# Optimization experiments

Hardware: AMD Instinct MI355X
Metric: run time of the kernel (lower is better)

## Reference

```python
import jax, jax.numpy as jnp
import numpy as np

N_NODES = 500000
N_EDGES = 5000000


def _sage_conv(x, edge_index, Wl, bl, Wr):
    # PyG SAGEConv (aggr='mean', root_weight=True):
    #   out = lin_l(mean_{j in N(i)} x_j) + lin_r(x_i)
    # edge_index[0] = source, edge_index[1] = target
    src, dst = edge_index[0], edge_index[1]
    n = x.shape[0]
    msg = x[src]  # [E, F] gather
    agg = jax.ops.segment_sum(msg, dst, num_segments=n)  # [N, F]
    deg = jax.ops.segment_sum(jnp.ones((src.shape[0],), x.dtype), dst, num_segments=n)
    agg = agg / jnp.maximum(deg, 1.0)[:, None]  # mean aggregation
    return agg @ Wl.T + bl + x @ Wr.T


def setup_inputs() -> dict:
    key = jax.random.key(0)
    k1, k2, k3, k4, k5, k6 = jax.random.split(key, 6)
    x = jax.random.normal(k1, (N_NODES, 2), dtype=jnp.float32)
    edge_index = jax.random.randint(k2, (2, N_EDGES), 0, N_NODES, dtype=jnp.int64)
    # conv1: SAGEConv(2, 16); conv2: SAGEConv(16, 1)
    s1 = 1.0 / np.sqrt(2.0)
    s2 = 1.0 / np.sqrt(16.0)
    W1l = jax.random.uniform(k3, (16, 2), jnp.float32, -s1, s1)
    W1r = jax.random.uniform(k4, (16, 2), jnp.float32, -s1, s1)
    b1 = jnp.zeros((16,), jnp.float32)
    W2l = jax.random.uniform(k5, (1, 16), jnp.float32, -s2, s2)
    W2r = jax.random.uniform(k6, (1, 16), jnp.float32, -s2, s2)
    b2 = jnp.zeros((1,), jnp.float32)
    return {"x": x, "edge_index": edge_index,
            "W1l": W1l, "b1": b1, "W1r": W1r,
            "W2l": W2l, "b2": b2, "W2r": W2r}


def reference(x, edge_index, W1l, b1, W1r, W2l, b2, W2r):
    h = jax.nn.relu(_sage_conv(x, edge_index, W1l, b1, W1r))  # [N, 16]
    h = _sage_conv(h, edge_index, W2l, b2, W2r)               # [N, 1]
    return jax.nn.sigmoid(h).squeeze(-1)                      # [N]
```

## Files before the change

kernel.cpp:

```cpp
#include <hip/hip_runtime.h>


static constexpr int ABLOCK = 512;
static constexpr int PBLOCK = 1024;
static constexpr int PGRID = 256;
static constexpr int BUCKET_BITS = 9;
static constexpr int BUCKET_NODES = 1 << BUCKET_BITS;
static constexpr int MAXNB = 1024;
static constexpr int CAP = 8192;
static constexpr int CSTRIDE = 16;
static constexpr int MAXCHUNK = 19584;

static constexpr float S1 = 65536.0f;
static constexpr float IS1 = 1.0f / 65536.0f;
static constexpr long long B1 = 8LL * 65536LL;
static constexpr float S2 = 16384.0f;
static constexpr float IS2 = 1.0f / 16384.0f;

__global__ __launch_bounds__(512) void k_init(unsigned* __restrict__ cursor, int NB) {
    int b = blockIdx.x * 512 + threadIdx.x;
    if (b < NB) cursor[(size_t)b * CSTRIDE] = (unsigned)b * (unsigned)CAP;
}

__global__ __launch_bounds__(PBLOCK) void k_part(
    const int* __restrict__ src, const int* __restrict__ dst,
    unsigned* __restrict__ cursor, unsigned* __restrict__ entries,
    int E, int NB)
{
    __shared__ unsigned sorted[MAXCHUNK];
    __shared__ unsigned hist[MAXNB];
    __shared__ unsigned loc[MAXNB];
    __shared__ unsigned base[MAXNB];
    const int tid = threadIdx.x;
    int chunk = ((E + (int)gridDim.x - 1) / (int)gridDim.x + 3) & ~3;
    const int e0 = blockIdx.x * chunk;
    const int e1 = min(e0 + chunk, E);
    const int n = max(0, e1 - e0);
    const int nv = n >> 2;
    const int4* dst4 = reinterpret_cast<const int4*>(dst + e0);
    const int4* src4 = reinterpret_cast<const int4*>(src + e0);

    for (int b = tid; b < MAXNB; b += PBLOCK) hist[b] = 0;
    __syncthreads();

    for (int t = tid; t < nv; t += PBLOCK) {
        int4 d = dst4[t];
        atomicAdd(&hist[(unsigned)d.x >> BUCKET_BITS], 1u);
        atomicAdd(&hist[(unsigned)d.y >> BUCKET_BITS], 1u);
        atomicAdd(&hist[(unsigned)d.z >> BUCKET_BITS], 1u);
        atomicAdd(&hist[(unsigned)d.w >> BUCKET_BITS], 1u);
    }
    for (int e = e0 + (nv << 2) + tid; e < e1; e += PBLOCK)
        atomicAdd(&hist[(unsigned)dst[e] >> BUCKET_BITS], 1u);
    __syncthreads();

    if (tid < NB) loc[tid] = hist[tid];
    __syncthreads();
    for (int off = 1; off < NB; off <<= 1) {
        unsigned v = 0;
        if (tid < NB && tid >= off) v = loc[tid - off];
        __syncthreads();
        if (tid < NB) loc[tid] += v;
        __syncthreads();
    }
    if (tid < NB) loc[tid] -= hist[tid];

    if (tid < NB) {
        int b = tid + (int)(blockIdx.x % (unsigned)NB);
        if (b >= NB) b -= NB;
        base[b] = atomicAdd(&cursor[(size_t)b * CSTRIDE], hist[b]);
    }
    __syncthreads();
    for (int b = tid; b < MAXNB; b += PBLOCK) hist[b] = 0;
    __syncthreads();

    for (int t = tid; t < nv; t += PBLOCK) {
        int4 d = dst4[t];
        int4 s = src4[t];
        {
            unsigned bk = (unsigned)d.x >> BUCKET_BITS;
            unsigned r = atomicAdd(&hist[bk], 1u);
            sorted[loc[bk] + r] = ((unsigned)s.x << BUCKET_BITS) | ((unsigned)d.x & (BUCKET_NODES - 1));
        }
        {
            unsigned bk = (unsigned)d.y >> BUCKET_BITS;
            unsigned r = atomicAdd(&hist[bk], 1u);
            sorted[loc[bk] + r] = ((unsigned)s.y << BUCKET_BITS) | ((unsigned)d.y & (BUCKET_NODES - 1));
        }
        {
            unsigned bk = (unsigned)d.z >> BUCKET_BITS;
            unsigned r = atomicAdd(&hist[bk], 1u);
            sorted[loc[bk] + r] = ((unsigned)s.z << BUCKET_BITS) | ((unsigned)d.z & (BUCKET_NODES - 1));
        }
        {
            unsigned bk = (unsigned)d.w >> BUCKET_BITS;
            unsigned r = atomicAdd(&hist[bk], 1u);
            sorted[loc[bk] + r] = ((unsigned)s.w << BUCKET_BITS) | ((unsigned)d.w & (BUCKET_NODES - 1));
        }
    }
    for (int e = e0 + (nv << 2) + tid; e < e1; e += PBLOCK) {
        unsigned d = (unsigned)dst[e];
        unsigned bk = d >> BUCKET_BITS;
        unsigned r = atomicAdd(&hist[bk], 1u);
        sorted[loc[bk] + r] = ((unsigned)src[e] << BUCKET_BITS) | (d & (BUCKET_NODES - 1));
    }
    __syncthreads();

    const int wave = tid >> 6, lane = tid & 63;
    const int nw = PBLOCK >> 6;
    const int off = (int)(blockIdx.x % (unsigned)NB);
    for (int j = wave; j < NB; j += nw) {
        int b = j + off;
        if (b >= NB) b -= NB;
        unsigned cnt = hist[b];
        if (cnt == 0) continue;
        unsigned lo = loc[b], ba = base[b];
        unsigned lim = (unsigned)(b + 1) * (unsigned)CAP;
        if (ba >= lim) continue;
        cnt = min(cnt, lim - ba);
        for (unsigned i = lane; i < cnt; i += 64)
            entries[ba + i] = sorted[lo + i];
    }
}

__global__ __launch_bounds__(ABLOCK) void k_agg1(
    const unsigned* __restrict__ entries, const unsigned* __restrict__ cursor,
    const float* __restrict__ x,
    const float* __restrict__ W1l, const float* __restrict__ b1,
    const float* __restrict__ W1r, const float* __restrict__ W2l,
    const float* __restrict__ W2r, const float* __restrict__ b2,
    unsigned* __restrict__ sq, float* __restrict__ t0a, float* __restrict__ ga,
    int N)
{
    __shared__ unsigned long long qs[BUCKET_NODES];
    int bk = blockIdx.x;
    for (int i = threadIdx.x; i < BUCKET_NODES; i += ABLOCK) qs[i] = 0ULL;
    __syncthreads();

    unsigned start = (unsigned)bk * (unsigned)CAP;
    unsigned end = min(cursor[(size_t)bk * CSTRIDE], start + (unsigned)CAP);
    unsigned n = end - start;
    unsigned nv = n >> 2;
    const uint4* e4 = reinterpret_cast<const uint4*>(entries + start);

    #define PROC1(en) { \
        unsigned s_ = (en) >> BUCKET_BITS; \
        unsigned dl_ = (en) & (BUCKET_NODES - 1); \
        float2 xv_ = *reinterpret_cast<const float2*>(x + 2 * (size_t)s_); \
        unsigned q0_ = (unsigned)__float2int_rn((xv_.x + 8.0f) * S1); \
        unsigned q1_ = (unsigned)__float2int_rn((xv_.y + 8.0f) * S1); \
        atomicAdd(&qs[dl_], (1ULL << 56) | ((unsigned long long)q0_ << 28) | (unsigned long long)q1_); }

    for (unsigned t = threadIdx.x; t < nv; t += ABLOCK) {
        uint4 en = e4[t];
        PROC1(en.x) PROC1(en.y) PROC1(en.z) PROC1(en.w)
    }
    for (unsigned t = start + (nv << 2) + threadIdx.x; t < end; t += ABLOCK) {
        unsigned en = entries[t];
        PROC1(en)
    }
    #undef PROC1
    __syncthreads();

    int nodebase = bk << BUCKET_BITS;
    for (int il = threadIdx.x; il < BUCKET_NODES; il += ABLOCK) {
        int i = nodebase + il;
        if (i >= N) continue;
        unsigned long long v = qs[il];
        int deg = (int)(v >> 56);
        long long q0 = (long long)((v >> 28) & 0xFFFFFFFULL);
        long long q1 = (long long)(v & 0xFFFFFFFULL);
        long long bias = (long long)deg * B1;
        float inv = 1.0f / (float)max(deg, 1);
        float m0 = (float)(q0 - bias) * IS1 * inv;
        float m1 = (float)(q1 - bias) * IS1 * inv;
        float2 xv = *reinterpret_cast<const float2*>(x + 2 * (size_t)i);
        float s = 0.0f, t0 = b2[0];
#pragma unroll
        for (int o = 0; o < 16; ++o) {
            float h = m0 * W1l[2 * o] + m1 * W1l[2 * o + 1] + b1[o]
                    + xv.x * W1r[2 * o] + xv.y * W1r[2 * o + 1];
            h = fmaxf(h, 0.0f);
            s  += h * W2l[o];
            t0 += h * W2r[o];
        }
        sq[i]  = (unsigned)__float2int_rn((s + 128.0f) * S2);
        t0a[i] = t0 - (deg > 0 ? 128.0f : 0.0f);
        ga[i]  = IS2 * inv;
    }
}

__global__ __launch_bounds__(ABLOCK) void k_agg2(
    const unsigned* __restrict__ entries, const unsigned* __restrict__ cursor,
    const unsigned* __restrict__ sq,
    const float* __restrict__ t0a, const float* __restrict__ ga,
    float* __restrict__ out, int N)
{
    __shared__ unsigned sbin[BUCKET_NODES];
    int bk = blockIdx.x;
    for (int i = threadIdx.x; i < BUCKET_NODES; i += ABLOCK) sbin[i] = 0;
    __syncthreads();

    unsigned start = (unsigned)bk * (unsigned)CAP;
    unsigned end = min(cursor[(size_t)bk * CSTRIDE], start + (unsigned)CAP);
    unsigned n = end - start;
    unsigned nv = n >> 2;
    const uint4* e4 = reinterpret_cast<const uint4*>(entries + start);

    #define PROC2(en) { \
        unsigned s_ = (en) >> BUCKET_BITS; \
        unsigned dl_ = (en) & (BUCKET_NODES - 1); \
        atomicAdd(&sbin[dl_], sq[s_]); }

    for (unsigned t = threadIdx.x; t < nv; t += ABLOCK) {
        uint4 en = e4[t];
        PROC2(en.x) PROC2(en.y) PROC2(en.z) PROC2(en.w)
    }
    for (unsigned t = start + (nv << 2) + threadIdx.x; t < end; t += ABLOCK) {
        unsigned en = entries[t];
        PROC2(en)
    }
    #undef PROC2
    __syncthreads();

    int nodebase = bk << BUCKET_BITS;
    for (int il = threadIdx.x; il < BUCKET_NODES; il += ABLOCK) {
        int i = nodebase + il;
        if (i >= N) continue;
        float t = (float)(int)sbin[il] * ga[i] + t0a[i];
        out[i] = 1.0f / (1.0f + expf(-t));
    }
}

__global__ __launch_bounds__(256) void k_scatter1_fb(
    const int* __restrict__ src, const int* __restrict__ dst,
    const float* __restrict__ x, float* __restrict__ agg1, float* __restrict__ deg, int E)
{
    int stride = gridDim.x * blockDim.x;
    for (int e = blockIdx.x * blockDim.x + threadIdx.x; e < E; e += stride) {
        int s = src[e], d = dst[e];
        float2 xv = *reinterpret_cast<const float2*>(x + 2 * (size_t)s);
        unsafeAtomicAdd(&agg1[2 * (size_t)d + 0], xv.x);
        unsafeAtomicAdd(&agg1[2 * (size_t)d + 1], xv.y);
        unsafeAtomicAdd(&deg[d], 1.0f);
    }
}
__global__ __launch_bounds__(256) void k_node1_fb(
    const float* __restrict__ x, const float* __restrict__ agg1, const float* __restrict__ deg,
    const float* __restrict__ W1l, const float* __restrict__ b1,
    const float* __restrict__ W1r, const float* __restrict__ W2l,
    float* __restrict__ sval, int N)
{
    int i = blockIdx.x * blockDim.x + threadIdx.x;
    if (i >= N) return;
    float inv = 1.0f / fmaxf(deg[i], 1.0f);
    float2 a = *reinterpret_cast<const float2*>(agg1 + 2 * (size_t)i);
    float m0 = a.x * inv, m1 = a.y * inv;
    float2 xv = *reinterpret_cast<const float2*>(x + 2 * (size_t)i);
    float s = 0.0f;
#pragma unroll
    for (int o = 0; o < 16; ++o) {
        float h = m0 * W1l[2 * o] + m1 * W1l[2 * o + 1] + b1[o]
                + xv.x * W1r[2 * o] + xv.y * W1r[2 * o + 1];
        s += fmaxf(h, 0.0f) * W2l[o];
    }
    sval[i] = s;
}
__global__ __launch_bounds__(256) void k_scatter2_fb(
    const int* __restrict__ src, const int* __restrict__ dst,
    const float* __restrict__ sval, float* __restrict__ agg_s, int E)
{
    int stride = gridDim.x * blockDim.x;
    for (int e = blockIdx.x * blockDim.x + threadIdx.x; e < E; e += stride)
        unsafeAtomicAdd(&agg_s[dst[e]], sval[src[e]]);
}
__global__ __launch_bounds__(256) void k_node2_fb(
    const float* __restrict__ x, const float* __restrict__ agg1, const float* __restrict__ deg,
    const float* __restrict__ agg_s,
    const float* __restrict__ W1l, const float* __restrict__ b1,
    const float* __restrict__ W1r, const float* __restrict__ W2r, const float* __restrict__ b2,
    float* __restrict__ out, int N)
{
    int i = blockIdx.x * blockDim.x + threadIdx.x;
    if (i >= N) return;
    float inv = 1.0f / fmaxf(deg[i], 1.0f);
    float2 a = *reinterpret_cast<const float2*>(agg1 + 2 * (size_t)i);
    float m0 = a.x * inv, m1 = a.y * inv;
    float2 xv = *reinterpret_cast<const float2*>(x + 2 * (size_t)i);
    float t = agg_s[i] * inv + b2[0];
#pragma unroll
    for (int o = 0; o < 16; ++o) {
        float h = m0 * W1l[2 * o] + m1 * W1l[2 * o + 1] + b1[o]
                + xv.x * W1r[2 * o] + xv.y * W1r[2 * o + 1];
        t += fmaxf(h, 0.0f) * W2r[o];
    }
    out[i] = 1.0f / (1.0f + expf(-t));
}

extern "C" void kernel_launch(void* const* d_in, const int* in_sizes, int n_in,
                              void* d_out, int out_size, void* d_ws, size_t ws_size,
                              hipStream_t stream) {
    const float* x   = (const float*)d_in[0];
    const int*   ei  = (const int*)d_in[1];
    const float* W1l = (const float*)d_in[2];
    const float* b1  = (const float*)d_in[3];
    const float* W1r = (const float*)d_in[4];
    const float* W2l = (const float*)d_in[5];
    const float* b2  = (const float*)d_in[6];
    const float* W2r = (const float*)d_in[7];

    const int N = in_sizes[0] / 2;
    const int E = in_sizes[1] / 2;
    const int* src = ei;
    const int* dst = ei + (size_t)E;
    float* out = (float*)d_out;

    const int NB = (N + BUCKET_NODES - 1) >> BUCKET_BITS;
    const int chunk = ((E + PGRID - 1) / PGRID + 3) & ~3;

    size_t needed = (size_t)MAXNB * CSTRIDE * 4 + (size_t)NB * CAP * 4 + 3 * (size_t)N * 4;
    if (NB <= MAXNB && chunk <= MAXCHUNK && ws_size >= needed) {
        unsigned* cursor  = (unsigned*)d_ws;
        unsigned* entries = cursor + (size_t)MAXNB * CSTRIDE;
        unsigned* sq      = entries + (size_t)NB * CAP;
        float*    t0a     = (float*)(sq + N);
        float*    ga      = t0a + N;

        k_init<<<(NB + 511) / 512, 512, 0, stream>>>(cursor, NB);
        k_part<<<PGRID, PBLOCK, 0, stream>>>(src, dst, cursor, entries, E, NB);
        k_agg1<<<NB, ABLOCK, 0, stream>>>(entries, cursor, x, W1l, b1, W1r, W2l, W2r, b2,
                                          sq, t0a, ga, N);
        k_agg2<<<NB, ABLOCK, 0, stream>>>(entries, cursor, sq, t0a, ga, out, N);
    } else {
        float* agg1  = (float*)d_ws;
        float* deg   = agg1 + 2 * (size_t)N;
        float* agg_s = deg + (size_t)N;
        float* sval  = agg_s + (size_t)N;
        hipMemsetAsync(d_ws, 0, 4 * (size_t)N * sizeof(float), stream);
        const int eblocks = 2048, nblocks = (N + 255) / 256;
        k_scatter1_fb<<<eblocks, 256, 0, stream>>>(src, dst, x, agg1, deg, E);
        k_node1_fb<<<nblocks, 256, 0, stream>>>(x, agg1, deg, W1l, b1, W1r, W2l, sval, N);
        k_scatter2_fb<<<eblocks, 256, 0, stream>>>(src, dst, sval, agg_s, E);
        k_node2_fb<<<nblocks, 256, 0, stream>>>(x, agg1, deg, agg_s, W1l, b1, W1r, W2r, b2, out, N);
    }
}
```

Measured before the change: 111.2 us.

## Fuse partition and both aggregation passes into one cooperative persistent kernel

Replaces the init, partition and two per-bucket aggregation kernels with a single cooperative kernel. The phases are separated by grid-wide syncs, and blocks pull buckets from global atomic tickets. Buckets grow from 512 to 1024 nodes so that one 1024-thread block covers a whole bucket. This removes launch gaps and inter-kernel drains. In exchange the aggregation phases run on only 256 resident blocks with one large LDS union each, which can lower occupancy, and the ticket scheme over 489 buckets can leave some blocks idle.

```diff
diff --git a/kernel.cpp b/kernel.cpp
--- a/kernel.cpp
+++ b/kernel.cpp
@@ -1,13 +1,15 @@
 #include <hip/hip_runtime.h>
-
-
-static constexpr int ABLOCK = 512;
-static constexpr int PBLOCK = 1024;
-static constexpr int PGRID = 256;
-static constexpr int BUCKET_BITS = 9;
+#include <hip/hip_cooperative_groups.h>
+
+namespace cg = cooperative_groups;
+
+
+static constexpr int TPB  = 1024;
+static constexpr int GRID = 256;
+static constexpr int BUCKET_BITS = 10;
 static constexpr int BUCKET_NODES = 1 << BUCKET_BITS;
-static constexpr int MAXNB = 1024;
-static constexpr int CAP = 8192;
+static constexpr int MAXNB = 512;
+static constexpr int CAP = 16384;
 static constexpr int CSTRIDE = 16;
 static constexpr int MAXCHUNK = 19584;
 
@@ -17,218 +19,239 @@
 static constexpr float S2 = 16384.0f;
 static constexpr float IS2 = 1.0f / 16384.0f;
 
-__global__ __launch_bounds__(512) void k_init(unsigned* __restrict__ cursor, int NB) {
-    int b = blockIdx.x * 512 + threadIdx.x;
-    if (b < NB) cursor[(size_t)b * CSTRIDE] = (unsigned)b * (unsigned)CAP;
-}
-
-__global__ __launch_bounds__(PBLOCK) void k_part(
+struct P1S {
+    unsigned sorted[MAXCHUNK];
+    unsigned hist[MAXNB];
+    unsigned loc[MAXNB];
+    unsigned base[MAXNB];
+};
+union SMU {
+    P1S p1;
+    unsigned long long qs[BUCKET_NODES];
+    unsigned sbin[BUCKET_NODES];
+};
+
+__global__ __launch_bounds__(TPB) void k_fused(
     const int* __restrict__ src, const int* __restrict__ dst,
-    unsigned* __restrict__ cursor, unsigned* __restrict__ entries,
-    int E, int NB)
-{
-    __shared__ unsigned sorted[MAXCHUNK];
-    __shared__ unsigned hist[MAXNB];
-    __shared__ unsigned loc[MAXNB];
-    __shared__ unsigned base[MAXNB];
-    const int tid = threadIdx.x;
-    int chunk = ((E + (int)gridDim.x - 1) / (int)gridDim.x + 3) & ~3;
-    const int e0 = blockIdx.x * chunk;
-    const int e1 = min(e0 + chunk, E);
-    const int n = max(0, e1 - e0);
-    const int nv = n >> 2;
-    const int4* dst4 = reinterpret_cast<const int4*>(dst + e0);
-    const int4* src4 = reinterpret_cast<const int4*>(src + e0);
-
-    for (int b = tid; b < MAXNB; b += PBLOCK) hist[b] = 0;
-    __syncthreads();
-
-    for (int t = tid; t < nv; t += PBLOCK) {
-        int4 d = dst4[t];
-        atomicAdd(&hist[(unsigned)d.x >> BUCKET_BITS], 1u);
-        atomicAdd(&hist[(unsigned)d.y >> BUCKET_BITS], 1u);
-        atomicAdd(&hist[(unsigned)d.z >> BUCKET_BITS], 1u);
-        atomicAdd(&hist[(unsigned)d.w >> BUCKET_BITS], 1u);
-    }
-    for (int e = e0 + (nv << 2) + tid; e < e1; e += PBLOCK)
-        atomicAdd(&hist[(unsigned)dst[e] >> BUCKET_BITS], 1u);
-    __syncthreads();
-
-    if (tid < NB) loc[tid] = hist[tid];
-    __syncthreads();
-    for (int off = 1; off < NB; off <<= 1) {
-        unsigned v = 0;
-        if (tid < NB && tid >= off) v = loc[tid - off];
-        __syncthreads();
-        if (tid < NB) loc[tid] += v;
-        __syncthreads();
-    }
-    if (tid < NB) loc[tid] -= hist[tid];
-
-    if (tid < NB) {
-        int b = tid + (int)(blockIdx.x % (unsigned)NB);
-        if (b >= NB) b -= NB;
-        base[b] = atomicAdd(&cursor[(size_t)b * CSTRIDE], hist[b]);
-    }
-    __syncthreads();
-    for (int b = tid; b < MAXNB; b += PBLOCK) hist[b] = 0;
-    __syncthreads();
-
-    for (int t = tid; t < nv; t += PBLOCK) {
-        int4 d = dst4[t];
-        int4 s = src4[t];
-        {
-            unsigned bk = (unsigned)d.x >> BUCKET_BITS;
-            unsigned r = atomicAdd(&hist[bk], 1u);
-            sorted[loc[bk] + r] = ((unsigned)s.x << BUCKET_BITS) | ((unsigned)d.x & (BUCKET_NODES - 1));
-        }
-        {
-            unsigned bk = (unsigned)d.y >> BUCKET_BITS;
-            unsigned r = atomicAdd(&hist[bk], 1u);
-            sorted[loc[bk] + r] = ((unsigned)s.y << BUCKET_BITS) | ((unsigned)d.y & (BUCKET_NODES - 1));
-        }
-        {
-            unsigned bk = (unsigned)d.z >> BUCKET_BITS;
-            unsigned r = atomicAdd(&hist[bk], 1u);
-            sorted[loc[bk] + r] = ((unsigned)s.z << BUCKET_BITS) | ((unsigned)d.z & (BUCKET_NODES - 1));
-        }
-        {
-            unsigned bk = (unsigned)d.w >> BUCKET_BITS;
-            unsigned r = atomicAdd(&hist[bk], 1u);
-            sorted[loc[bk] + r] = ((unsigned)s.w << BUCKET_BITS) | ((unsigned)d.w & (BUCKET_NODES - 1));
-        }
-    }
-    for (int e = e0 + (nv << 2) + tid; e < e1; e += PBLOCK) {
-        unsigned d = (unsigned)dst[e];
-        unsigned bk = d >> BUCKET_BITS;
-        unsigned r = atomicAdd(&hist[bk], 1u);
-        sorted[loc[bk] + r] = ((unsigned)src[e] << BUCKET_BITS) | (d & (BUCKET_NODES - 1));
-    }
-    __syncthreads();
-
-    const int wave = tid >> 6, lane = tid & 63;
-    const int nw = PBLOCK >> 6;
-    const int off = (int)(blockIdx.x % (unsigned)NB);
-    for (int j = wave; j < NB; j += nw) {
-        int b = j + off;
-        if (b >= NB) b -= NB;
-        unsigned cnt = hist[b];
-        if (cnt == 0) continue;
-        unsigned lo = loc[b], ba = base[b];
-        unsigned lim = (unsigned)(b + 1) * (unsigned)CAP;
-        if (ba >= lim) continue;
-        cnt = min(cnt, lim - ba);
-        for (unsigned i = lane; i < cnt; i += 64)
-            entries[ba + i] = sorted[lo + i];
-    }
-}
-
-__global__ __launch_bounds__(ABLOCK) void k_agg1(
-    const unsigned* __restrict__ entries, const unsigned* __restrict__ cursor,
     const float* __restrict__ x,
     const float* __restrict__ W1l, const float* __restrict__ b1,
     const float* __restrict__ W1r, const float* __restrict__ W2l,
-    const float* __restrict__ W2r, const float* __restrict__ b2,
+    const float* __restrict__ b2,  const float* __restrict__ W2r,
+    unsigned* __restrict__ cursor, unsigned* __restrict__ tickets,
+    unsigned* __restrict__ entries,
     unsigned* __restrict__ sq, float* __restrict__ t0a, float* __restrict__ ga,
-    int N)
-{
-    __shared__ unsigned long long qs[BUCKET_NODES];
-    int bk = blockIdx.x;
-    for (int i = threadIdx.x; i < BUCKET_NODES; i += ABLOCK) qs[i] = 0ULL;
-    __syncthreads();
-
-    unsigned start = (unsigned)bk * (unsigned)CAP;
-    unsigned end = min(cursor[(size_t)bk * CSTRIDE], start + (unsigned)CAP);
-    unsigned n = end - start;
-    unsigned nv = n >> 2;
-    const uint4* e4 = reinterpret_cast<const uint4*>(entries + start);
-
-    #define PROC1(en) { \
-        unsigned s_ = (en) >> BUCKET_BITS; \
-        unsigned dl_ = (en) & (BUCKET_NODES - 1); \
-        float2 xv_ = *reinterpret_cast<const float2*>(x + 2 * (size_t)s_); \
-        unsigned q0_ = (unsigned)__float2int_rn((xv_.x + 8.0f) * S1); \
-        unsigned q1_ = (unsigned)__float2int_rn((xv_.y + 8.0f) * S1); \
-        atomicAdd(&qs[dl_], (1ULL << 56) | ((unsigned long long)q0_ << 28) | (unsigned long long)q1_); }
-
-    for (unsigned t = threadIdx.x; t < nv; t += ABLOCK) {
-        uint4 en = e4[t];
-        PROC1(en.x) PROC1(en.y) PROC1(en.z) PROC1(en.w)
-    }
-    for (unsigned t = start + (nv << 2) + threadIdx.x; t < end; t += ABLOCK) {
-        unsigned en = entries[t];
-        PROC1(en)
-    }
-    #undef PROC1
-    __syncthreads();
-
-    int nodebase = bk << BUCKET_BITS;
-    for (int il = threadIdx.x; il < BUCKET_NODES; il += ABLOCK) {
-        int i = nodebase + il;
-        if (i >= N) continue;
-        unsigned long long v = qs[il];
-        int deg = (int)(v >> 56);
-        long long q0 = (long long)((v >> 28) & 0xFFFFFFFULL);
-        long long q1 = (long long)(v & 0xFFFFFFFULL);
-        long long bias = (long long)deg * B1;
-        float inv = 1.0f / (float)max(deg, 1);
-        float m0 = (float)(q0 - bias) * IS1 * inv;
-        float m1 = (float)(q1 - bias) * IS1 * inv;
-        float2 xv = *reinterpret_cast<const float2*>(x + 2 * (size_t)i);
-        float s = 0.0f, t0 = b2[0];
+    float* __restrict__ out,
+    int E, int N, int NB)
+{
+    __shared__ SMU sm;
+    __shared__ unsigned sm_cur;
+    cg::grid_group grid = cg::this_grid();
+    const int tid = threadIdx.x;
+
+    if (blockIdx.x == 0) {
+        for (int b = tid; b < NB; b += TPB)
+            cursor[(size_t)b * CSTRIDE] = (unsigned)b * (unsigned)CAP;
+        if (tid < 2) tickets[(size_t)tid * CSTRIDE] = 0u;
+    }
+    grid.sync();
+
+    {
+        const int chunk = ((E + GRID - 1) / GRID + 3) & ~3;
+        const int e0 = (int)blockIdx.x * chunk;
+        const int e1 = min(e0 + chunk, E);
+        const int n  = max(0, e1 - e0);
+        const int nv = n >> 2;
+        const int4* dst4 = reinterpret_cast<const int4*>(dst + e0);
+        const int4* src4 = reinterpret_cast<const int4*>(src + e0);
+
+        for (int b = tid; b < MAXNB; b += TPB) sm.p1.hist[b] = 0;
+        __syncthreads();
+
+        for (int t = tid; t < nv; t += TPB) {
+            int4 d = dst4[t];
+            atomicAdd(&sm.p1.hist[(unsigned)d.x >> BUCKET_BITS], 1u);
+            atomicAdd(&sm.p1.hist[(unsigned)d.y >> BUCKET_BITS], 1u);
+            atomicAdd(&sm.p1.hist[(unsigned)d.z >> BUCKET_BITS], 1u);
+            atomicAdd(&sm.p1.hist[(unsigned)d.w >> BUCKET_BITS], 1u);
+        }
+        for (int e = e0 + (nv << 2) + tid; e < e1; e += TPB)
+            atomicAdd(&sm.p1.hist[(unsigned)dst[e] >> BUCKET_BITS], 1u);
+        __syncthreads();
+
+        if (tid < NB) sm.p1.loc[tid] = sm.p1.hist[tid];
+        __syncthreads();
+        for (int off = 1; off < NB; off <<= 1) {
+            unsigned v = 0;
+            if (tid < NB && tid >= off) v = sm.p1.loc[tid - off];
+            __syncthreads();
+            if (tid < NB) sm.p1.loc[tid] += v;
+            __syncthreads();
+        }
+        if (tid < NB) sm.p1.loc[tid] -= sm.p1.hist[tid];
+
+        if (tid < NB) {
+            int b = tid + (int)(blockIdx.x % (unsigned)NB);
+            if (b >= NB) b -= NB;
+            sm.p1.base[b] = atomicAdd(&cursor[(size_t)b * CSTRIDE], sm.p1.hist[b]);
+        }
+        __syncthreads();
+        for (int b = tid; b < MAXNB; b += TPB) sm.p1.hist[b] = 0;
+        __syncthreads();
+
+        for (int t = tid; t < nv; t += TPB) {
+            int4 d = dst4[t];
+            int4 s = src4[t];
+            {
+                unsigned bk = (unsigned)d.x >> BUCKET_BITS;
+                unsigned r = atomicAdd(&sm.p1.hist[bk], 1u);
+                sm.p1.sorted[sm.p1.loc[bk] + r] =
+                    ((unsigned)s.x << BUCKET_BITS) | ((unsigned)d.x & (BUCKET_NODES - 1));
+            }
+            {
+                unsigned bk = (unsigned)d.y >> BUCKET_BITS;
+                unsigned r = atomicAdd(&sm.p1.hist[bk], 1u);
+                sm.p1.sorted[sm.p1.loc[bk] + r] =
+                    ((unsigned)s.y << BUCKET_BITS) | ((unsigned)d.y & (BUCKET_NODES - 1));
+            }
+            {
+                unsigned bk = (unsigned)d.z >> BUCKET_BITS;
+                unsigned r = atomicAdd(&sm.p1.hist[bk], 1u);
+                sm.p1.sorted[sm.p1.loc[bk] + r] =
+                    ((unsigned)s.z << BUCKET_BITS) | ((unsigned)d.z & (BUCKET_NODES - 1));
+            }
+            {
+                unsigned bk = (unsigned)d.w >> BUCKET_BITS;
+                unsigned r = atomicAdd(&sm.p1.hist[bk], 1u);
+                sm.p1.sorted[sm.p1.loc[bk] + r] =
+                    ((unsigned)s.w << BUCKET_BITS) | ((unsigned)d.w & (BUCKET_NODES - 1));
+            }
+        }
+        for (int e = e0 + (nv << 2) + tid; e < e1; e += TPB) {
+            unsigned d = (unsigned)dst[e];
+            unsigned bk = d >> BUCKET_BITS;
+            unsigned r = atomicAdd(&sm.p1.hist[bk], 1u);
+            sm.p1.sorted[sm.p1.loc[bk] + r] =
+                ((unsigned)src[e] << BUCKET_BITS) | (d & (BUCKET_NODES - 1));
+        }
+        __syncthreads();
+
+        const int wave = tid >> 6, lane = tid & 63;
+        const int nw = TPB >> 6;
+        const int off = (int)(blockIdx.x % (unsigned)NB);
+        for (int j = wave; j < NB; j += nw) {
+            int b = j + off;
+            if (b >= NB) b -= NB;
+            unsigned cnt = sm.p1.hist[b];
+            if (cnt == 0) continue;
+            unsigned lo = sm.p1.loc[b], ba = sm.p1.base[b];
+            unsigned lim = (unsigned)(b + 1) * (unsigned)CAP;
+            if (ba >= lim) continue;
+            cnt = min(cnt, lim - ba);
+            for (unsigned i = lane; i < cnt; i += 64)
+                entries[ba + i] = sm.p1.sorted[lo + i];
+        }
+    }
+    grid.sync();
+
+    while (true) {
+        __syncthreads();
+        if (tid == 0) sm_cur = atomicAdd(&tickets[0], 1u);
+        __syncthreads();
+        unsigned bk = sm_cur;
+        if (bk >= (unsigned)NB) break;
+
+        sm.qs[tid] = 0ULL;
+        __syncthreads();
+
+        unsigned start = bk * (unsigned)CAP;
+        unsigned end = min(cursor[(size_t)bk * CSTRIDE], start + (unsigned)CAP);
+        unsigned n = end - start;
+        unsigned nv = n >> 2;
+        const uint4* e4 = reinterpret_cast<const uint4*>(entries + start);
+
+        #define PROC1(en) { \
+            unsigned s_ = (en) >> BUCKET_BITS; \
+            unsigned dl_ = (en) & (BUCKET_NODES - 1); \
+            float2 xv_ = *reinterpret_cast<const float2*>(x + 2 * (size_t)s_); \
+            unsigned q0_ = (unsigned)__float2int_rn((xv_.x + 8.0f) * S1); \
+            unsigned q1_ = (unsigned)__float2int_rn((xv_.y + 8.0f) * S1); \
+            atomicAdd(&sm.qs[dl_], (1ULL << 56) | ((unsigned long long)q0_ << 28) | (unsigned long long)q1_); }
+
+        for (unsigned t = tid; t < nv; t += TPB) {
+            uint4 en = e4[t];
+            PROC1(en.x) PROC1(en.y) PROC1(en.z) PROC1(en.w)
+        }
+        for (unsigned t = start + (nv << 2) + tid; t < end; t += TPB) {
+            unsigned en = entries[t];
+            PROC1(en)
+        }
+        #undef PROC1
+        __syncthreads();
+
+        int i = (int)(bk << BUCKET_BITS) + tid;
+        if (i < N) {
+            unsigned long long v = sm.qs[tid];
+            int deg = (int)(v >> 56);
+            long long q0 = (long long)((v >> 28) & 0xFFFFFFFULL);
+            long long q1 = (long long)(v & 0xFFFFFFFULL);
+            long long bias = (long long)deg * B1;
+            float inv = 1.0f / (float)max(deg, 1);
+            float m0 = (float)(q0 - bias) * IS1 * inv;
+            float m1 = (float)(q1 - bias) * IS1 * inv;
+            float2 xv = *reinterpret_cast<const float2*>(x + 2 * (size_t)i);
+            float s = 0.0f, t0 = b2[0];
 #pragma unroll
-        for (int o = 0; o < 16; ++o) {
-            float h = m0 * W1l[2 * o] + m1 * W1l[2 * o + 1] + b1[o]
-                    + xv.x * W1r[2 * o] + xv.y * W1r[2 * o + 1];
-            h = fmaxf(h, 0.0f);
-            s  += h * W2l[o];
-            t0 += h * W2r[o];
-        }
-        sq[i]  = (unsigned)__float2int_rn((s + 128.0f) * S2);
-        t0a[i] = t0 - (deg > 0 ? 128.0f : 0.0f);
-        ga[i]  = IS2 * inv;
-    }
-}
-
-__global__ __launch_bounds__(ABLOCK) void k_agg2(
-    const unsigned* __restrict__ entries, const unsigned* __restrict__ cursor,
-    const unsigned* __restrict__ sq,
-    const float* __restrict__ t0a, const float* __restrict__ ga,
-    float* __restrict__ out, int N)
-{
-    __shared__ unsigned sbin[BUCKET_NODES];
-    int bk = blockIdx.x;
-    for (int i = threadIdx.x; i < BUCKET_NODES; i += ABLOCK) sbin[i] = 0;
-    __syncthreads();
-
-    unsigned start = (unsigned)bk * (unsigned)CAP;
-    unsigned end = min(cursor[(size_t)bk * CSTRIDE], start + (unsigned)CAP);
-    unsigned n = end - start;
-    unsigned nv = n >> 2;
-    const uint4* e4 = reinterpret_cast<const uint4*>(entries + start);
-
-    #define PROC2(en) { \
-        unsigned s_ = (en) >> BUCKET_BITS; \
-        unsigned dl_ = (en) & (BUCKET_NODES - 1); \
-        atomicAdd(&sbin[dl_], sq[s_]); }
-
-    for (unsigned t = threadIdx.x; t < nv; t += ABLOCK) {
-        uint4 en = e4[t];
-        PROC2(en.x) PROC2(en.y) PROC2(en.z) PROC2(en.w)
-    }
-    for (unsigned t = start + (nv << 2) + threadIdx.x; t < end; t += ABLOCK) {
-        unsigned en = entries[t];
-        PROC2(en)
-    }
-    #undef PROC2
-    __syncthreads();
-
-    int nodebase = bk << BUCKET_BITS;
-    for (int il = threadIdx.x; il < BUCKET_NODES; il += ABLOCK) {
-        int i = nodebase + il;
-        if (i >= N) continue;
-        float t = (float)(int)sbin[il] * ga[i] + t0a[i];
-        out[i] = 1.0f / (1.0f + expf(-t));
+            for (int o = 0; o < 16; ++o) {
+                float h = m0 * W1l[2 * o] + m1 * W1l[2 * o + 1] + b1[o]
+                        + xv.x * W1r[2 * o] + xv.y * W1r[2 * o + 1];
+                h = fmaxf(h, 0.0f);
+                s  += h * W2l[o];
+                t0 += h * W2r[o];
+            }
+            sq[i]  = (unsigned)__float2int_rn((s + 128.0f) * S2);
+            t0a[i] = t0 - (deg > 0 ? 128.0f : 0.0f);
+            ga[i]  = IS2 * inv;
+        }
+    }
+    grid.sync();
+
+    while (true) {
+        __syncthreads();
+        if (tid == 0) sm_cur = atomicAdd(&tickets[(size_t)CSTRIDE], 1u);
+        __syncthreads();
+        unsigned bk = sm_cur;
+        if (bk >= (unsigned)NB) break;
+
+        sm.sbin[tid] = 0u;
+        __syncthreads();
+
+        unsigned start = bk * (unsigned)CAP;
+        unsigned end = min(cursor[(size_t)bk * CSTRIDE], start + (unsigned)CAP);
+        unsigned n = end - start;
+        unsigned nv = n >> 2;
+        const uint4* e4 = reinterpret_cast<const uint4*>(entries + start);
+
+        #define PROC2(en) { \
+            unsigned s_ = (en) >> BUCKET_BITS; \
+            unsigned dl_ = (en) & (BUCKET_NODES - 1); \
+            atomicAdd(&sm.sbin[dl_], sq[s_]); }
+
+        for (unsigned t = tid; t < nv; t += TPB) {
+            uint4 en = e4[t];
+            PROC2(en.x) PROC2(en.y) PROC2(en.z) PROC2(en.w)
+        }
+        for (unsigned t = start + (nv << 2) + tid; t < end; t += TPB) {
+            unsigned en = entries[t];
+            PROC2(en)
+        }
+        #undef PROC2
+        __syncthreads();
+
+        int i = (int)(bk << BUCKET_BITS) + tid;
+        if (i < N) {
+            float t = (float)(int)sm.sbin[tid] * ga[i] + t0a[i];
+            out[i] = 1.0f / (1.0f + expf(-t));
+        }
     }
 }
 
@@ -297,50 +320,69 @@
     out[i] = 1.0f / (1.0f + expf(-t));
 }
 
+static void launch_fallback(const int* src, const int* dst, const float* x,
+                            const float* W1l, const float* b1, const float* W1r,
+                            const float* W2l, const float* b2, const float* W2r,
+                            float* out, void* d_ws, int N, int E, hipStream_t stream)
+{
+    float* agg1  = (float*)d_ws;
+    float* deg   = agg1 + 2 * (size_t)N;
+    float* agg_s = deg + (size_t)N;
+    float* sval  = agg_s + (size_t)N;
+    hipMemsetAsync(d_ws, 0, 4 * (size_t)N * sizeof(float), stream);
+    const int eblocks = 2048, nblocks = (N + 255) / 256;
+    k_scatter1_fb<<<eblocks, 256, 0, stream>>>(src, dst, x, agg1, deg, E);
+    k_node1_fb<<<nblocks, 256, 0, stream>>>(x, agg1, deg, W1l, b1, W1r, W2l, sval, N);
+    k_scatter2_fb<<<eblocks, 256, 0, stream>>>(src, dst, sval, agg_s, E);
+    k_node2_fb<<<nblocks, 256, 0, stream>>>(x, agg1, deg, agg_s, W1l, b1, W1r, W2r, b2, out, N);
+}
+
 extern "C" void kernel_launch(void* const* d_in, const int* in_sizes, int n_in,
                               void* d_out, int out_size, void* d_ws, size_t ws_size,
                               hipStream_t stream) {
-    const float* x   = (const float*)d_in[0];
-    const int*   ei  = (const int*)d_in[1];
-    const float* W1l = (const float*)d_in[2];
-    const float* b1  = (const float*)d_in[3];
-    const float* W1r = (const float*)d_in[4];
-    const float* W2l = (const float*)d_in[5];
-    const float* b2  = (const float*)d_in[6];
-    const float* W2r = (const float*)d_in[7];
-
-    const int N = in_sizes[0] / 2;
-    const int E = in_sizes[1] / 2;
-    const int* src = ei;
-    const int* dst = ei + (size_t)E;
+    const int* srcp   = (const int*)d_in[1];
+    const float* x    = (const float*)d_in[0];
+    const float* W1l  = (const float*)d_in[2];
+    const float* b1   = (const float*)d_in[3];
+    const float* W1r  = (const float*)d_in[4];
+    const float* W2l  = (const float*)d_in[5];
+    const float* b2   = (const float*)d_in[6];
+    const float* W2r  = (const float*)d_in[7];
+
+    int N = in_sizes[0] / 2;
+    int E = in_sizes[1] / 2;
+    const int* src = srcp;
+    const int* dst = srcp + (size_t)E;
     float* out = (float*)d_out;
 
-    const int NB = (N + BUCKET_NODES - 1) >> BUCKET_BITS;
-    const int chunk = ((E + PGRID - 1) / PGRID + 3) & ~3;
-
-    size_t needed = (size_t)MAXNB * CSTRIDE * 4 + (size_t)NB * CAP * 4 + 3 * (size_t)N * 4;
-    if (NB <= MAXNB && chunk <= MAXCHUNK && ws_size >= needed) {
+    int NB = (N + BUCKET_NODES - 1) >> BUCKET_BITS;
+    const int chunk = ((E + GRID - 1) / GRID + 3) & ~3;
+
+    size_t needed = (size_t)MAXNB * CSTRIDE * 4 + 64 * 4
+                  + (size_t)NB * CAP * 4 + 3 * (size_t)N * 4;
+    if (NB <= MAXNB && NB <= TPB && chunk <= MAXCHUNK && ws_size >= needed) {
         unsigned* cursor  = (unsigned*)d_ws;
-        unsigned* entries = cursor + (size_t)MAXNB * CSTRIDE;
+        unsigned* tickets = cursor + (size_t)MAXNB * CSTRIDE;
+        unsigned* entries = tickets + 64;
         unsigned* sq      = entries + (size_t)NB * CAP;
         float*    t0a     = (float*)(sq + N);
         float*    ga      = t0a + N;
 
-        k_init<<<(NB + 511) / 512, 512, 0, stream>>>(cursor, NB);
-        k_part<<<PGRID, PBLOCK, 0, stream>>>(src, dst, cursor, entries, E, NB);
-        k_agg1<<<NB, ABLOCK, 0, stream>>>(entries, cursor, x, W1l, b1, W1r, W2l, W2r, b2,
-                                          sq, t0a, ga, N);
-        k_agg2<<<NB, ABLOCK, 0, stream>>>(entries, cursor, sq, t0a, ga, out, N);
+        void* args[] = {
+            (void*)&src, (void*)&dst, (void*)&x,
+            (void*)&W1l, (void*)&b1, (void*)&W1r, (void*)&W2l,
+            (void*)&b2, (void*)&W2r,
+            (void*)&cursor, (void*)&tickets, (void*)&entries,
+            (void*)&sq, (void*)&t0a, (void*)&ga, (void*)&out,
+            (void*)&E, (void*)&N, (void*)&NB
+        };
+        hipError_t err = hipLaunchCooperativeKernel(
+            (const void*)k_fused, dim3(GRID), dim3(TPB), args, 0, stream);
+        if (err != hipSuccess)
+            launch_fallback(src, dst, x, W1l, b1, W1r, W2l, b2, W2r,
+                            out, d_ws, N, E, stream);
     } else {
-        float* agg1  = (float*)d_ws;
-        float* deg   = agg1 + 2 * (size_t)N;
-        float* agg_s = deg + (size_t)N;
-        float* sval  = agg_s + (size_t)N;
-        hipMemsetAsync(d_ws, 0, 4 * (size_t)N * sizeof(float), stream);
-        const int eblocks = 2048, nblocks = (N + 255) / 256;
-        k_scatter1_fb<<<eblocks, 256, 0, stream>>>(src, dst, x, agg1, deg, E);
-        k_node1_fb<<<nblocks, 256, 0, stream>>>(x, agg1, deg, W1l, b1, W1r, W2l, sval, N);
-        k_scatter2_fb<<<eblocks, 256, 0, stream>>>(src, dst, sval, agg_s, E);
-        k_node2_fb<<<nblocks, 256, 0, stream>>>(x, agg1, deg, agg_s, W1l, b1, W1r, W2r, b2, out, N);
-    }
-}
+        launch_fallback(src, dst, x, W1l, b1, W1r, W2l, b2, W2r,
+                        out, d_ws, N, E, stream);
+    }
+}
```

After: 179.8 us. 61.6% more time.

## Preload partition edges into registers and double bucket width

Applied to the files above, without the earlier changes.

The partition kernel now gives each block a fixed chunk of edges and loads them all into registers up front. Both the histogram pass and the scatter pass read from those registers instead of re-reading global memory, which raises memory-level parallelism and removes the second load of the edges. Buckets grow from 512 to 1024 nodes with a larger per-bucket capacity, so there are half as many buckets and aggregation blocks. Both aggregation loops get an unroll hint. The trade-off is more register pressure in the partition kernel and fewer, heavier aggregation blocks, which may leave some compute units underused.

```diff
diff --git a/kernel.cpp b/kernel.cpp
--- a/kernel.cpp
+++ b/kernel.cpp
@@ -3,13 +3,13 @@
 
 static constexpr int ABLOCK = 512;
 static constexpr int PBLOCK = 1024;
-static constexpr int PGRID = 256;
-static constexpr int BUCKET_BITS = 9;
+static constexpr int KITER  = 5;
+static constexpr int CHUNK  = PBLOCK * 4 * KITER;
+static constexpr int BUCKET_BITS = 10;
 static constexpr int BUCKET_NODES = 1 << BUCKET_BITS;
-static constexpr int MAXNB = 1024;
-static constexpr int CAP = 8192;
+static constexpr int MAXNB = 512;
+static constexpr int CAP = 16384;
 static constexpr int CSTRIDE = 16;
-static constexpr int MAXCHUNK = 19584;
 
 static constexpr float S1 = 65536.0f;
 static constexpr float IS1 = 1.0f / 65536.0f;
@@ -27,31 +27,47 @@
     unsigned* __restrict__ cursor, unsigned* __restrict__ entries,
     int E, int NB)
 {
-    __shared__ unsigned sorted[MAXCHUNK];
+    __shared__ unsigned sorted[CHUNK];
     __shared__ unsigned hist[MAXNB];
     __shared__ unsigned loc[MAXNB];
     __shared__ unsigned base[MAXNB];
     const int tid = threadIdx.x;
-    int chunk = ((E + (int)gridDim.x - 1) / (int)gridDim.x + 3) & ~3;
-    const int e0 = blockIdx.x * chunk;
-    const int e1 = min(e0 + chunk, E);
-    const int n = max(0, e1 - e0);
-    const int nv = n >> 2;
+    const int e0 = (int)blockIdx.x * CHUNK;
+    const int e1 = min(e0 + CHUNK, E);
     const int4* dst4 = reinterpret_cast<const int4*>(dst + e0);
     const int4* src4 = reinterpret_cast<const int4*>(src + e0);
 
+    int4 dR[KITER], sR[KITER];
+#pragma unroll
+    for (int k = 0; k < KITER; ++k) {
+        int g = tid + k * PBLOCK;
+        int e = e0 + 4 * g;
+        if (e + 3 < e1) {
+            dR[k] = dst4[g];
+            sR[k] = src4[g];
+        } else {
+            dR[k] = make_int4(-1, -1, -1, -1);
+            sR[k] = make_int4(0, 0, 0, 0);
+#pragma unroll
+            for (int j = 0; j < 4; ++j) {
+                if (e + j < e1) {
+                    (&dR[k].x)[j] = dst[e + j];
+                    (&sR[k].x)[j] = src[e + j];
+                }
+            }
+        }
+    }
+
     for (int b = tid; b < MAXNB; b += PBLOCK) hist[b] = 0;
     __syncthreads();
 
-    for (int t = tid; t < nv; t += PBLOCK) {
-        int4 d = dst4[t];
-        atomicAdd(&hist[(unsigned)d.x >> BUCKET_BITS], 1u);
-        atomicAdd(&hist[(unsigned)d.y >> BUCKET_BITS], 1u);
-        atomicAdd(&hist[(unsigned)d.z >> BUCKET_BITS], 1u);
-        atomicAdd(&hist[(unsigned)d.w >> BUCKET_BITS], 1u);
-    }
-    for (int e = e0 + (nv << 2) + tid; e < e1; e += PBLOCK)
-        atomicAdd(&hist[(unsigned)dst[e] >> BUCKET_BITS], 1u);
+    #define HIST1(dv) { unsigned du_ = (unsigned)(dv); \
+        if (du_ != 0xFFFFFFFFu) atomicAdd(&hist[du_ >> BUCKET_BITS], 1u); }
+#pragma unroll
+    for (int k = 0; k < KITER; ++k) {
+        HIST1(dR[k].x) HIST1(dR[k].y) HIST1(dR[k].z) HIST1(dR[k].w)
+    }
+    #undef HIST1
     __syncthreads();
 
     if (tid < NB) loc[tid] = hist[tid];
@@ -74,36 +90,17 @@
     for (int b = tid; b < MAXNB; b += PBLOCK) hist[b] = 0;
     __syncthreads();
 
-    for (int t = tid; t < nv; t += PBLOCK) {
-        int4 d = dst4[t];
-        int4 s = src4[t];
-        {
-            unsigned bk = (unsigned)d.x >> BUCKET_BITS;
-            unsigned r = atomicAdd(&hist[bk], 1u);
-            sorted[loc[bk] + r] = ((unsigned)s.x << BUCKET_BITS) | ((unsigned)d.x & (BUCKET_NODES - 1));
-        }
-        {
-            unsigned bk = (unsigned)d.y >> BUCKET_BITS;
-            unsigned r = atomicAdd(&hist[bk], 1u);
-            sorted[loc[bk] + r] = ((unsigned)s.y << BUCKET_BITS) | ((unsigned)d.y & (BUCKET_NODES - 1));
-        }
-        {
-            unsigned bk = (unsigned)d.z >> BUCKET_BITS;
-            unsigned r = atomicAdd(&hist[bk], 1u);
-            sorted[loc[bk] + r] = ((unsigned)s.z << BUCKET_BITS) | ((unsigned)d.z & (BUCKET_NODES - 1));
-        }
-        {
-            unsigned bk = (unsigned)d.w >> BUCKET_BITS;
-            unsigned r = atomicAdd(&hist[bk], 1u);
-            sorted[loc[bk] + r] = ((unsigned)s.w << BUCKET_BITS) | ((unsigned)d.w & (BUCKET_NODES - 1));
-        }
-    }
-    for (int e = e0 + (nv << 2) + tid; e < e1; e += PBLOCK) {
-        unsigned d = (unsigned)dst[e];
-        unsigned bk = d >> BUCKET_BITS;
-        unsigned r = atomicAdd(&hist[bk], 1u);
-        sorted[loc[bk] + r] = ((unsigned)src[e] << BUCKET_BITS) | (d & (BUCKET_NODES - 1));
-    }
+    #define SCAT1(dv, sv) { unsigned du_ = (unsigned)(dv); \
+        if (du_ != 0xFFFFFFFFu) { \
+            unsigned bk_ = du_ >> BUCKET_BITS; \
+            unsigned r_ = atomicAdd(&hist[bk_], 1u); \
+            sorted[loc[bk_] + r_] = ((unsigned)(sv) << BUCKET_BITS) | (du_ & (BUCKET_NODES - 1)); } }
+#pragma unroll
+    for (int k = 0; k < KITER; ++k) {
+        SCAT1(dR[k].x, sR[k].x) SCAT1(dR[k].y, sR[k].y)
+        SCAT1(dR[k].z, sR[k].z) SCAT1(dR[k].w, sR[k].w)
+    }
+    #undef SCAT1
     __syncthreads();
 
     const int wave = tid >> 6, lane = tid & 63;
@@ -151,6 +148,7 @@
         unsigned q1_ = (unsigned)__float2int_rn((xv_.y + 8.0f) * S1); \
         atomicAdd(&qs[dl_], (1ULL << 56) | ((unsigned long long)q0_ << 28) | (unsigned long long)q1_); }
 
+#pragma unroll 2
     for (unsigned t = threadIdx.x; t < nv; t += ABLOCK) {
         uint4 en = e4[t];
         PROC1(en.x) PROC1(en.y) PROC1(en.z) PROC1(en.w)
@@ -212,6 +210,7 @@
         unsigned dl_ = (en) & (BUCKET_NODES - 1); \
         atomicAdd(&sbin[dl_], sq[s_]); }
 
+#pragma unroll 2
     for (unsigned t = threadIdx.x; t < nv; t += ABLOCK) {
         uint4 en = e4[t];
         PROC2(en.x) PROC2(en.y) PROC2(en.z) PROC2(en.w)
@@ -316,10 +315,10 @@
     float* out = (float*)d_out;
 
     const int NB = (N + BUCKET_NODES - 1) >> BUCKET_BITS;
-    const int chunk = ((E + PGRID - 1) / PGRID + 3) & ~3;
+    const int pblocks = (E + CHUNK - 1) / CHUNK;
 
     size_t needed = (size_t)MAXNB * CSTRIDE * 4 + (size_t)NB * CAP * 4 + 3 * (size_t)N * 4;
-    if (NB <= MAXNB && chunk <= MAXCHUNK && ws_size >= needed) {
+    if (NB <= MAXNB && NB <= PBLOCK && ws_size >= needed) {
         unsigned* cursor  = (unsigned*)d_ws;
         unsigned* entries = cursor + (size_t)MAXNB * CSTRIDE;
         unsigned* sq      = entries + (size_t)NB * CAP;
@@ -327,7 +326,7 @@
         float*    ga      = t0a + N;
 
         k_init<<<(NB + 511) / 512, 512, 0, stream>>>(cursor, NB);
-        k_part<<<PGRID, PBLOCK, 0, stream>>>(src, dst, cursor, entries, E, NB);
+        k_part<<<pblocks, PBLOCK, 0, stream>>>(src, dst, cursor, entries, E, NB);
         k_agg1<<<NB, ABLOCK, 0, stream>>>(entries, cursor, x, W1l, b1, W1r, W2l, W2r, b2,
                                           sq, t0a, ga, N);
         k_agg2<<<NB, ABLOCK, 0, stream>>>(entries, cursor, sq, t0a, ga, out, N);
```

New measurement: 98.20 us. 1.13x faster.
